# Performance work log

Measured on AMD Instinct MI355X. Metric: run time of the kernel, lower is better.

Reference implementation:

```python
import jax, jax.numpy as jnp
import numpy as np
from jax import lax

B, C1, C2, OUT, H, W = 8, 256, 128, 256, 64, 64
MID = max(C1, C2)
D = max(MID // 8, 4)

def conv1x1(x, w, b=None):
    # x: [B,C,H,W], w: [O,C]
    y = jnp.einsum('bchw,oc->bohw', x, w)
    if b is not None:
        y = y + b[None, :, None, None]
    return y

def dwconv3x3(x, w, b):
    # depthwise 3x3, padding=1; w: [C,1,3,3]
    y = lax.conv_general_dilated(x, w, (1, 1), 'SAME',
                                 dimension_numbers=('NCHW', 'OIHW', 'NCHW'),
                                 feature_group_count=x.shape[1])
    return y + b[None, :, None, None]

def setup_inputs() -> dict:
    key = jax.random.key(0)
    ks = jax.random.split(key, 16)
    def w1x1(k, o, i):
        return jax.random.normal(k, (o, i), jnp.float32) * np.sqrt(2.0 / o)
    def wdw(k, c):
        return jax.random.normal(k, (c, 1, 3, 3), jnp.float32) * np.sqrt(2.0 / (9 * c))
    z = lambda c: jnp.zeros((c,), jnp.float32)
    return {
        'x1': jax.random.normal(ks[0], (B, C1, H, W), jnp.float32),
        'x2': jax.random.normal(ks[1], (B, C2, H, W), jnp.float32),
        'conv_r_w': w1x1(ks[2], MID, C1), 'conv_r_b': z(MID),
        'conv_n_w': w1x1(ks[3], MID, C2), 'conv_n_b': z(MID),
        'mlp_w1': w1x1(ks[4], D, MID),
        'mlp_w2': w1x1(ks[5], 2 * MID, D),
        'pq_w': w1x1(ks[6], MID, MID), 'pq_b': z(MID),
        'dq_w': wdw(ks[7], MID), 'dq_b': z(MID),
        'pk_w': w1x1(ks[8], MID, MID), 'pk_b': z(MID),
        'dk_w': wdw(ks[9], MID), 'dk_b': z(MID),
        'pv_w': w1x1(ks[10], MID, MID), 'pv_b': z(MID),
        'dv_w': wdw(ks[11], MID), 'dv_b': z(MID),
        'out_w': w1x1(ks[12], OUT, MID), 'out_b': z(OUT),
        'alpha': jnp.float32(1.0),
        'lambd': jnp.float32(0.5),
        'beta': jnp.float32(0.5),
    }

def reference(x1, x2, conv_r_w, conv_r_b, conv_n_w, conv_n_b, mlp_w1, mlp_w2,
              pq_w, pq_b, dq_w, dq_b, pk_w, pk_b, dk_w, dk_b,
              pv_w, pv_b, dv_w, dv_b, out_w, out_b, alpha, lambd, beta):
    FR = conv1x1(x1, conv_r_w, conv_r_b)          # [B,C,H,W]
    FN = conv1x1(x2, conv_n_w, conv_n_b)          # [B,C,H,W]
    stack = jnp.stack([FR, FN], axis=1)           # [B,2,C,H,W]
    feats_sum = FR + FN
    pooled = feats_sum.mean(axis=(2, 3))          # [B,C] (adaptive avg pool 1x1)
    h = jax.nn.relu(jnp.einsum('bc,dc->bd', pooled, mlp_w1))
    a = jnp.einsum('bd,ed->be', h, mlp_w2).reshape(B, 2, MID)
    attn = jax.nn.softmax(a, axis=1)              # softmax over the 2 branches
    Fw = jnp.einsum('bkchw,bkc->bchw', stack, attn)
    Q = dwconv3x3(conv1x1(Fw, pq_w, pq_b), dq_w, dq_b)
    K = dwconv3x3(conv1x1(Fw, pk_w, pk_b), dk_w, dk_b)
    V = dwconv3x3(conv1x1(Fw, pv_w, pv_b), dv_w, dv_b)
    FQ = jnp.fft.fft2(Q.astype(jnp.float32), axes=(-2, -1))   # complex64 [B,C,H,W]
    FK = jnp.fft.fft2(K.astype(jnp.float32), axes=(-2, -1))
    elem = (FQ * FK).reshape(B, MID, H * W)                    # [B,C,HW]
    FQf = FQ.reshape(B, MID, H * W)
    FKf = FK.reshape(B, MID, H * W)
    attn_matrix = jnp.einsum('bcn,bdn->bcd', FQf, FKf)         # complex [B,C,C]
    attn_w = jax.nn.softmax(jnp.abs(attn_matrix) / alpha, axis=-1)
    attn_wc = attn_w.astype(jnp.complex64)
    F_CFR = jnp.einsum('bcd,bdn->bcn', attn_wc, elem).reshape(B, MID, H, W)
    cfr = jnp.real(jnp.fft.ifft2(F_CFR, axes=(-2, -1))).astype(Q.dtype)
    F_DFR = V - lambd * V * cfr
    freq_out = Q * cfr + F_DFR
    output = beta * freq_out + (1.0 - beta) * Fw
    return conv1x1(output, out_w, out_b)
```

## Files before the change

kernel.cpp:

```cpp
#include <hip/hip_runtime.h>
#include <math.h>

#ifndef M_PI
#define M_PI 3.14159265358979323846
#endif

typedef unsigned int u32;

constexpr int  NB   = 8;
constexpr int  CH   = 256;
constexpr long HW   = 4096;
constexpr long SLOT = (long)NB * CH * HW;
constexpr int  SPLITK = 8;
constexpr long ST   = (long)CH * HW;

__device__ __forceinline__ float rne_hi(float x) {
  unsigned u = __float_as_uint(x);
  unsigned r = (u + 0x7FFFu + ((u >> 16) & 1u)) & 0xFFFF0000u;
  return __uint_as_float(r);
}
__device__ __forceinline__ u32 packf(float x) {
  const float h = rne_hi(x);
  const float l = x - h;
  return (__float_as_uint(h) & 0xFFFF0000u) | (__float_as_uint(l) >> 16);
}
__device__ __forceinline__ float unpackf(u32 u) {
  return __uint_as_float(u & 0xFFFF0000u) + __uint_as_float(u << 16);
}
__device__ __forceinline__ unsigned bfpair(float x, float y) {
  return (__float_as_uint(x) >> 16) | (__float_as_uint(y) & 0xFFFF0000u);
}

typedef short bf16x8 __attribute__((ext_vector_type(8)));
typedef float f32x4  __attribute__((ext_vector_type(4)));

__global__ __launch_bounds__(256)
void cvt_kernel(const float* __restrict__ src, u32* __restrict__ dst, int n4)
{
  const int i = blockIdx.x * 256 + threadIdx.x;
  if (i < n4) {
    const float4 v = ((const float4*)src)[i];
    uint4 o;
    o.x = packf(v.x); o.y = packf(v.y); o.z = packf(v.z); o.w = packf(v.w);
    ((uint4*)dst)[i] = o;
  }
}

template<bool BPACKED, int EPI>
__global__ __launch_bounds__(256)
void gemm_mfma(const u32* __restrict__ A, const void* __restrict__ Bv,
               void* __restrict__ Cv, const float* __restrict__ bias,
               int K, long aStride, long bStride, long cStride,
               const u32* __restrict__ qb, const u32* __restrict__ vb,
               const u32* __restrict__ fwb,
               const float* __restrict__ lambd, const float* __restrict__ beta)
{
  constexpr int N = 4096;
  __shared__ __align__(16) unsigned short sAh[128 * 48];
  __shared__ __align__(16) unsigned short sAl[128 * 48];
  __shared__ __align__(16) unsigned short sBh[128 * 48];
  __shared__ __align__(16) unsigned short sBl[128 * 48];

  const int tid = threadIdx.x;
  const int b   = blockIdx.z;
  const int m0  = blockIdx.y * 128;
  const int n0  = blockIdx.x * 128;
  const u32* Ab = A + (long)b * aStride;

  const int ar = tid >> 1;
  const int ak = (tid & 1) * 16;
  const int aBase = ar * 48 + ak;
  const int bn = tid & 127;
  const int bk = (tid >> 7) * 16;
  const int bBase = bn * 48 + bk;

  const int wv = tid >> 6, lane = tid & 63;
  const int wy = wv >> 1, wx = wv & 1;
  const int quad = lane >> 4, l15 = lane & 15;

  f32x4 acc[4][4];
#pragma unroll
  for (int i = 0; i < 4; ++i)
#pragma unroll
    for (int j = 0; j < 4; ++j) acc[i][j] = (f32x4){0.f, 0.f, 0.f, 0.f};

  u32   ra[16];
  u32   rbu[16];
  float rbf[16];
  {
    const u32* ap = Ab + (long)(m0 + ar) * K + ak;
#pragma unroll
    for (int i = 0; i < 4; ++i) {
      const uint4 t = *(const uint4*)(ap + i * 4);
      ra[4*i] = t.x; ra[4*i+1] = t.y; ra[4*i+2] = t.z; ra[4*i+3] = t.w;
    }
    if (BPACKED) {
      const u32* bp = (const u32*)Bv + (long)b * bStride + (long)bk * N + n0 + bn;
#pragma unroll
      for (int i = 0; i < 16; ++i) rbu[i] = bp[(long)i * N];
    } else {
      const float* bp = (const float*)Bv + (long)b * bStride + (long)bk * N + n0 + bn;
#pragma unroll
      for (int i = 0; i < 16; ++i) rbf[i] = bp[(long)i * N];
    }
  }

  for (int kt = 0; kt < K; kt += 32) {
    {
      u32 hi[8], lo[8];
#pragma unroll
      for (int e = 0; e < 8; ++e) {
        const u32 u0 = ra[2*e], u1 = ra[2*e+1];
        hi[e] = (u0 >> 16) | (u1 & 0xFFFF0000u);
        lo[e] = (u0 & 0xFFFFu) | (u1 << 16);
      }
      *(uint4*)&sAh[aBase]     = make_uint4(hi[0], hi[1], hi[2], hi[3]);
      *(uint4*)&sAh[aBase + 8] = make_uint4(hi[4], hi[5], hi[6], hi[7]);
      *(uint4*)&sAl[aBase]     = make_uint4(lo[0], lo[1], lo[2], lo[3]);
      *(uint4*)&sAl[aBase + 8] = make_uint4(lo[4], lo[5], lo[6], lo[7]);
    }
    if (BPACKED) {
      u32 hi[8], lo[8];
#pragma unroll
      for (int e = 0; e < 8; ++e) {
        const u32 u0 = rbu[2*e], u1 = rbu[2*e+1];
        hi[e] = (u0 >> 16) | (u1 & 0xFFFF0000u);
        lo[e] = (u0 & 0xFFFFu) | (u1 << 16);
      }
      *(uint4*)&sBh[bBase]     = make_uint4(hi[0], hi[1], hi[2], hi[3]);
      *(uint4*)&sBh[bBase + 8] = make_uint4(hi[4], hi[5], hi[6], hi[7]);
      *(uint4*)&sBl[bBase]     = make_uint4(lo[0], lo[1], lo[2], lo[3]);
      *(uint4*)&sBl[bBase + 8] = make_uint4(lo[4], lo[5], lo[6], lo[7]);
    } else {
      float h[16], l[16];
#pragma unroll
      for (int e = 0; e < 16; ++e) { h[e] = rne_hi(rbf[e]); l[e] = rbf[e] - h[e]; }
      *(uint4*)&sBh[bBase]     = make_uint4(bfpair(h[0],h[1]), bfpair(h[2],h[3]),
                                            bfpair(h[4],h[5]), bfpair(h[6],h[7]));
      *(uint4*)&sBh[bBase + 8] = make_uint4(bfpair(h[8],h[9]), bfpair(h[10],h[11]),
                                            bfpair(h[12],h[13]), bfpair(h[14],h[15]));
      *(uint4*)&sBl[bBase]     = make_uint4(bfpair(l[0],l[1]), bfpair(l[2],l[3]),
                                            bfpair(l[4],l[5]), bfpair(l[6],l[7]));
      *(uint4*)&sBl[bBase + 8] = make_uint4(bfpair(l[8],l[9]), bfpair(l[10],l[11]),
                                            bfpair(l[12],l[13]), bfpair(l[14],l[15]));
    }
    __syncthreads();

    if (kt + 32 < K) {
      const u32* ap = Ab + (long)(m0 + ar) * K + kt + 32 + ak;
#pragma unroll
      for (int i = 0; i < 4; ++i) {
        const uint4 t = *(const uint4*)(ap + i * 4);
        ra[4*i] = t.x; ra[4*i+1] = t.y; ra[4*i+2] = t.z; ra[4*i+3] = t.w;
      }
      if (BPACKED) {
        const u32* bp = (const u32*)Bv + (long)b * bStride + (long)(kt + 32 + bk) * N + n0 + bn;
#pragma unroll
        for (int i = 0; i < 16; ++i) rbu[i] = bp[(long)i * N];
      } else {
        const float* bp = (const float*)Bv + (long)b * bStride + (long)(kt + 32 + bk) * N + n0 + bn;
#pragma unroll
        for (int i = 0; i < 16; ++i) rbf[i] = bp[(long)i * N];
      }
    }

    bf16x8 ah[4], al[4];
#pragma unroll
    for (int i = 0; i < 4; ++i) {
      const int idx = (wy * 64 + i * 16 + l15) * 48 + quad * 8;
      ah[i] = *(const bf16x8*)&sAh[idx];
      al[i] = *(const bf16x8*)&sAl[idx];
    }
#pragma unroll
    for (int j = 0; j < 4; ++j) {
      const int idx = (wx * 64 + j * 16 + l15) * 48 + quad * 8;
      const bf16x8 bh = *(const bf16x8*)&sBh[idx];
      const bf16x8 bl = *(const bf16x8*)&sBl[idx];
#pragma unroll
      for (int i = 0; i < 4; ++i) {
        acc[i][j] = __builtin_amdgcn_mfma_f32_16x16x32_bf16(ah[i], bh, acc[i][j], 0, 0, 0);
        acc[i][j] = __builtin_amdgcn_mfma_f32_16x16x32_bf16(ah[i], bl, acc[i][j], 0, 0, 0);
        acc[i][j] = __builtin_amdgcn_mfma_f32_16x16x32_bf16(al[i], bh, acc[i][j], 0, 0, 0);
      }
    }
    __syncthreads();
  }

  if (EPI == 0) {
    float* Cb = (float*)Cv + (long)b * cStride;
#pragma unroll
    for (int i = 0; i < 4; ++i)
#pragma unroll
      for (int r = 0; r < 4; ++r) {
        const int row = m0 + wy * 64 + i * 16 + quad * 4 + r;
        const float bb = bias ? bias[row] : 0.f;
#pragma unroll
        for (int j = 0; j < 4; ++j) {
          const int col = n0 + wx * 64 + j * 16 + l15;
          Cb[(long)row * N + col] = acc[i][j][r] + bb;
        }
      }
  } else if (EPI == 1) {
    u32* Cb = (u32*)Cv + (long)b * cStride;
#pragma unroll
    for (int i = 0; i < 4; ++i)
#pragma unroll
      for (int r = 0; r < 4; ++r) {
        const int row = m0 + wy * 64 + i * 16 + quad * 4 + r;
        const float bb = bias ? bias[row] : 0.f;
#pragma unroll
        for (int j = 0; j < 4; ++j) {
          const int col = n0 + wx * 64 + j * 16 + l15;
          Cb[(long)row * N + col] = packf(acc[i][j][r] + bb);
        }
      }
  } else {
    u32* Cb = (u32*)Cv + (long)b * cStride;
    const float lam = lambd[0], bet = beta[0];
#pragma unroll
    for (int i = 0; i < 4; ++i)
#pragma unroll
      for (int r = 0; r < 4; ++r) {
        const int row = m0 + wy * 64 + i * 16 + quad * 4 + r;
#pragma unroll
        for (int j = 0; j < 4; ++j) {
          const int col = n0 + wx * 64 + j * 16 + l15;
          const long off = (long)row * N + col;
          const long gi  = (long)b * cStride + off;
          const float q = unpackf(qb[gi]);
          const float v = unpackf(vb[gi]);
          const float f = unpackf(fwb[gi]);
          Cb[off] = packf(bet * (acc[i][j][r] * (q - lam * v) + v) + (1.f - bet) * f);
        }
      }
  }
}

__global__ __launch_bounds__(256)
void gemm_logits(const u32* __restrict__ Q, const u32* __restrict__ Kr,
                 float* __restrict__ Lp)
{
  __shared__ __align__(16) unsigned short sAh[128 * 48];
  __shared__ __align__(16) unsigned short sAl[128 * 48];
  __shared__ __align__(16) unsigned short sBh[128 * 48];
  __shared__ __align__(16) unsigned short sBl[128 * 48];

  const int tid = threadIdx.x;
  const int bz  = blockIdx.z;
  const int b   = bz >> 3, sp = bz & 7;
  const int m0  = blockIdx.y * 128;
  const int n0  = blockIdx.x * 128;
  const long k0b = (long)sp * 512;

  const int ar = tid >> 1;
  const int ak = (tid & 1) * 16;
  const int aBase = ar * 48 + ak;

  const int wv = tid >> 6, lane = tid & 63;
  const int wy = wv >> 1, wx = wv & 1;
  const int quad = lane >> 4, l15 = lane & 15;

  f32x4 acc[4][4];
#pragma unroll
  for (int i = 0; i < 4; ++i)
#pragma unroll
    for (int j = 0; j < 4; ++j) acc[i][j] = (f32x4){0.f, 0.f, 0.f, 0.f};

  const u32* Abase = Q  + (long)b * ST + (long)(m0 + ar) * 4096 + k0b + ak;
  const u32* Bbase = Kr + (long)b * ST + (long)(n0 + ar) * 4096 + k0b + ak;

  u32 ra[16], rb[16];
#pragma unroll
  for (int i = 0; i < 4; ++i) {
    uint4 t = *(const uint4*)(Abase + i * 4);
    ra[4*i] = t.x; ra[4*i+1] = t.y; ra[4*i+2] = t.z; ra[4*i+3] = t.w;
    t = *(const uint4*)(Bbase + i * 4);
    rb[4*i] = t.x; rb[4*i+1] = t.y; rb[4*i+2] = t.z; rb[4*i+3] = t.w;
  }

  for (int kt = 0; kt < 512; kt += 32) {
    {
      u32 hi[8], lo[8];
#pragma unroll
      for (int e = 0; e < 8; ++e) {
        const u32 u0 = ra[2*e], u1 = ra[2*e+1];
        hi[e] = (u0 >> 16) | (u1 & 0xFFFF0000u);
        lo[e] = (u0 & 0xFFFFu) | (u1 << 16);
      }
      *(uint4*)&sAh[aBase]     = make_uint4(hi[0], hi[1], hi[2], hi[3]);
      *(uint4*)&sAh[aBase + 8] = make_uint4(hi[4], hi[5], hi[6], hi[7]);
      *(uint4*)&sAl[aBase]     = make_uint4(lo[0], lo[1], lo[2], lo[3]);
      *(uint4*)&sAl[aBase + 8] = make_uint4(lo[4], lo[5], lo[6], lo[7]);
#pragma unroll
      for (int e = 0; e < 8; ++e) {
        const u32 u0 = rb[2*e], u1 = rb[2*e+1];
        hi[e] = (u0 >> 16) | (u1 & 0xFFFF0000u);
        lo[e] = (u0 & 0xFFFFu) | (u1 << 16);
      }
      *(uint4*)&sBh[aBase]     = make_uint4(hi[0], hi[1], hi[2], hi[3]);
      *(uint4*)&sBh[aBase + 8] = make_uint4(hi[4], hi[5], hi[6], hi[7]);
      *(uint4*)&sBl[aBase]     = make_uint4(lo[0], lo[1], lo[2], lo[3]);
      *(uint4*)&sBl[aBase + 8] = make_uint4(lo[4], lo[5], lo[6], lo[7]);
    }
    __syncthreads();

    if (kt + 32 < 512) {
#pragma unroll
      for (int i = 0; i < 4; ++i) {
        uint4 t = *(const uint4*)(Abase + kt + 32 + i * 4);
        ra[4*i] = t.x; ra[4*i+1] = t.y; ra[4*i+2] = t.z; ra[4*i+3] = t.w;
        t = *(const uint4*)(Bbase + kt + 32 + i * 4);
        rb[4*i] = t.x; rb[4*i+1] = t.y; rb[4*i+2] = t.z; rb[4*i+3] = t.w;
      }
    }

    bf16x8 ah[4], al[4];
#pragma unroll
    for (int i = 0; i < 4; ++i) {
      const int idx = (wy * 64 + i * 16 + l15) * 48 + quad * 8;
      ah[i] = *(const bf16x8*)&sAh[idx];
      al[i] = *(const bf16x8*)&sAl[idx];
    }
#pragma unroll
    for (int j = 0; j < 4; ++j) {
      const int idx = (wx * 64 + j * 16 + l15) * 48 + quad * 8;
      const bf16x8 bh = *(const bf16x8*)&sBh[idx];
      const bf16x8 bl = *(const bf16x8*)&sBl[idx];
#pragma unroll
      for (int i = 0; i < 4; ++i) {
        acc[i][j] = __builtin_amdgcn_mfma_f32_16x16x32_bf16(ah[i], bh, acc[i][j], 0, 0, 0);
        acc[i][j] = __builtin_amdgcn_mfma_f32_16x16x32_bf16(ah[i], bl, acc[i][j], 0, 0, 0);
        acc[i][j] = __builtin_amdgcn_mfma_f32_16x16x32_bf16(al[i], bh, acc[i][j], 0, 0, 0);
      }
    }
    __syncthreads();
  }

  float* Lb = Lp + (long)bz * 65536;
#pragma unroll
  for (int i = 0; i < 4; ++i)
#pragma unroll
    for (int r = 0; r < 4; ++r) {
      const int row = m0 + wy * 64 + i * 16 + quad * 4 + r;
#pragma unroll
      for (int j = 0; j < 4; ++j) {
        const int col = n0 + wx * 64 + j * 16 + l15;
        Lb[(long)row * 256 + col] = acc[i][j][r];
      }
    }
}

__global__ __launch_bounds__(256)
void pool_kernel(const u32* __restrict__ FR, const u32* __restrict__ FN,
                 float* __restrict__ pooled)
{
  __shared__ float red[256];
  const int bc = blockIdx.x, tid = threadIdx.x;
  const uint4* a = (const uint4*)(FR + (long)bc * HW);
  const uint4* b = (const uint4*)(FN + (long)bc * HW);
  float s = 0.f;
  for (int v = tid; v < 1024; v += 256) {
    const uint4 x = a[v];
    s += unpackf(x.x) + unpackf(x.y) + unpackf(x.z) + unpackf(x.w);
    const uint4 y = b[v];
    s += unpackf(y.x) + unpackf(y.y) + unpackf(y.z) + unpackf(y.w);
  }
  red[tid] = s; __syncthreads();
  for (int o = 128; o > 0; o >>= 1) {
    if (tid < o) red[tid] += red[tid + o];
    __syncthreads();
  }
  if (tid == 0) pooled[bc] = red[0] * (1.f / 4096.f);
}

__global__ __launch_bounds__(256)
void attn2_kernel(const float* __restrict__ pooled, const float* __restrict__ w1,
                  const float* __restrict__ w2, float* __restrict__ attn2)
{
  __shared__ float ps[256];
  __shared__ float hs[32];
  const int b = blockIdx.x, tid = threadIdx.x;
  ps[tid] = pooled[b * 256 + tid];
  __syncthreads();
  if (tid < 32) {
    float a = 0.f;
    for (int c = 0; c < 256; ++c) a += ps[c] * w1[tid * 256 + c];
    hs[tid] = fmaxf(a, 0.f);
  }
  __syncthreads();
  float a0 = 0.f, a1 = 0.f;
  for (int d = 0; d < 32; ++d) {
    const float h = hs[d];
    a0 += h * w2[tid * 32 + d];
    a1 += h * w2[(256 + tid) * 32 + d];
  }
  const float m  = fmaxf(a0, a1);
  const float e0 = expf(a0 - m), e1 = expf(a1 - m);
  const float inv = 1.f / (e0 + e1);
  attn2[b * 512 + tid]       = e0 * inv;
  attn2[b * 512 + 256 + tid] = e1 * inv;
}

__global__ __launch_bounds__(256)
void fw_kernel(const u32* __restrict__ FR, const u32* __restrict__ FN,
               const float* __restrict__ attn2, u32* __restrict__ FW)
{
  const int b = blockIdx.z, c = blockIdx.y;
  const float a0 = attn2[b * 512 + c];
  const float a1 = attn2[b * 512 + 256 + c];
  const long base4 = ((long)b * 256 + c) * 1024;
  const int i = blockIdx.x * 256 + threadIdx.x;
  const uint4 r = ((const uint4*)FR)[base4 + i];
  const uint4 n = ((const uint4*)FN)[base4 + i];
  uint4 o;
  o.x = packf(a0 * unpackf(r.x) + a1 * unpackf(n.x));
  o.y = packf(a0 * unpackf(r.y) + a1 * unpackf(n.y));
  o.z = packf(a0 * unpackf(r.z) + a1 * unpackf(n.z));
  o.w = packf(a0 * unpackf(r.w) + a1 * unpackf(n.w));
  ((uint4*)FW)[base4 + i] = o;
}

__global__ __launch_bounds__(256)
void dw_kernel(const u32* __restrict__ in, const float* __restrict__ w,
               const float* __restrict__ bias, u32* __restrict__ out,
               u32* __restrict__ out_rev)
{
  __shared__ float img[66][66];
  const int bc = blockIdx.x, tid = threadIdx.x;
  const int c = bc & 255;
  for (int v = tid; v < 66 * 66; v += 256) ((float*)img)[v] = 0.f;
  __syncthreads();
  const uint4* in4 = (const uint4*)(in + (long)bc * HW);
  for (int v = tid; v < 1024; v += 256) {
    const uint4 x = in4[v];
    const int r = v >> 4, c0 = ((v & 15) << 2) + 1;
    img[r + 1][c0 + 0] = unpackf(x.x);
    img[r + 1][c0 + 1] = unpackf(x.y);
    img[r + 1][c0 + 2] = unpackf(x.z);
    img[r + 1][c0 + 3] = unpackf(x.w);
  }
  float wr[9];
#pragma unroll
  for (int j = 0; j < 9; ++j) wr[j] = w[c * 9 + j];
  const float bb = bias[c];
  __syncthreads();
  for (int p = tid; p < 4096; p += 256) {
    const int y = p >> 6, x = p & 63;
    float s = bb;
#pragma unroll
    for (int ky = 0; ky < 3; ++ky)
#pragma unroll
      for (int kx = 0; kx < 3; ++kx)
        s = fmaf(wr[ky * 3 + kx], img[y + ky][x + kx], s);
    const u32 u = packf(s);
    out[(long)bc * HW + p] = u;
    if (out_rev)
      out_rev[(long)bc * HW + (((64 - y) & 63) << 6) + ((64 - x) & 63)] = u;
  }
}

#define SWA(r, c) (((r) << 6) | ((c) ^ (r)))
#define REV6(x)   ((((x) & 3) << 4) | ((x) & 12) | ((x) >> 4))

__device__ __forceinline__ float2 cmul(float2 a, float2 w) {
  return make_float2(a.x * w.x - a.y * w.y, a.x * w.y + a.y * w.x);
}
__device__ __forceinline__ float2 cmulc(float2 a, float2 w) {
  return make_float2(a.x * w.x + a.y * w.y, a.y * w.x - a.x * w.y);
}

__device__ __forceinline__ void fft_fwd(float2* __restrict__ Z,
                                        const float2* __restrict__ twt, int tid)
{
  const int lane = tid & 63;
  const int kb   = tid >> 6;
  for (int pass = 0; pass < 2; ++pass) {
    for (int s = 0; s < 3; ++s) {
      const int h  = 1 << (2 * s);
      const int us = 16 >> (2 * s);
#pragma unroll
      for (int q = 0; q < 4; ++q) {
        const int k = kb + 4 * q;
        const int j = k & (h - 1);
        const int g = k >> (2 * s);
        const int bse = g * 4 * h + j;
        const int p0 = bse, p1 = bse + h, p2 = bse + 2 * h, p3 = bse + 3 * h;
        const int a0 = pass ? SWA(p0, lane) : SWA(lane, p0);
        const int a1 = pass ? SWA(p1, lane) : SWA(lane, p1);
        const int a2 = pass ? SWA(p2, lane) : SWA(lane, p2);
        const int a3 = pass ? SWA(p3, lane) : SWA(lane, p3);
        float2 x0 = Z[a0];
        float2 x1 = Z[a1];
        float2 x2 = Z[a2];
        float2 x3 = Z[a3];
        const int e = j * us;
        x1 = cmul(x1, twt[e & 63]);
        x2 = cmul(x2, twt[(2 * e) & 63]);
        x3 = cmul(x3, twt[(3 * e) & 63]);
        const float2 t0 = make_float2(x0.x + x2.x, x0.y + x2.y);
        const float2 t1 = make_float2(x0.x - x2.x, x0.y - x2.y);
        const float2 t2 = make_float2(x1.x + x3.x, x1.y + x3.y);
        const float2 t3 = make_float2(x1.x - x3.x, x1.y - x3.y);
        Z[a0] = make_float2(t0.x + t2.x, t0.y + t2.y);
        Z[a2] = make_float2(t0.x - t2.x, t0.y - t2.y);
        Z[a1] = make_float2(t1.x + t3.y, t1.y - t3.x);
        Z[a3] = make_float2(t1.x - t3.y, t1.y + t3.x);
      }
      __syncthreads();
    }
  }
}

__device__ __forceinline__ void fft_inv(float2* __restrict__ Z,
                                        const float2* __restrict__ twt, int tid)
{
  const int lane = tid & 63;
  const int kb   = tid >> 6;
  for (int pass = 0; pass < 2; ++pass) {
    for (int s = 2; s >= 0; --s) {
      const int h  = 1 << (2 * s);
      const int us = 16 >> (2 * s);
#pragma unroll
      for (int q = 0; q < 4; ++q) {
        const int k = kb + 4 * q;
        const int j = k & (h - 1);
        const int g = k >> (2 * s);
        const int bse = g * 4 * h + j;
        const int p0 = bse, p1 = bse + h, p2 = bse + 2 * h, p3 = bse + 3 * h;
        const int a0 = pass ? SWA(lane, p0) : SWA(p0, lane);
        const int a1 = pass ? SWA(lane, p1) : SWA(p1, lane);
        const int a2 = pass ? SWA(lane, p2) : SWA(p2, lane);
        const int a3 = pass ? SWA(lane, p3) : SWA(p3, lane);
        const float2 x0 = Z[a0];
        const float2 x1 = Z[a1];
        const float2 x2 = Z[a2];
        const float2 x3 = Z[a3];
        const float2 t0 = make_float2(x0.x + x2.x, x0.y + x2.y);
        const float2 t1 = make_float2(x0.x - x2.x, x0.y - x2.y);
        const float2 t2 = make_float2(x1.x + x3.x, x1.y + x3.y);
        const float2 t3 = make_float2(x1.x - x3.x, x1.y - x3.y);
        const float2 y0 = make_float2(t0.x + t2.x, t0.y + t2.y);
        float2 y2 = make_float2(t0.x - t2.x, t0.y - t2.y);
        float2 y1 = make_float2(t1.x - t3.y, t1.y + t3.x);
        float2 y3 = make_float2(t1.x + t3.y, t1.y - t3.x);
        const int e = j * us;
        y1 = cmulc(y1, twt[e & 63]);
        y2 = cmulc(y2, twt[(2 * e) & 63]);
        y3 = cmulc(y3, twt[(3 * e) & 63]);
        Z[a0] = y0;
        Z[a1] = y1;
        Z[a2] = y2;
        Z[a3] = y3;
      }
      __syncthreads();
    }
  }
}

__global__ __launch_bounds__(256, 4)
void sconv_kernel(const u32* __restrict__ Qg, const u32* __restrict__ Kg,
                  u32* __restrict__ Sg)
{
  __shared__ float2 Z[4096];
  __shared__ float2 twt[64];
  const int tid = threadIdx.x;
  const long base = (long)blockIdx.x * 4096;
  if (tid < 64) {
    float sn, cs;
    __sincosf(-2.f * (float)M_PI * (float)tid * (1.f / 64.f), &sn, &cs);
    twt[tid] = make_float2(cs, sn);
  }

  {
    const uint4* Q4 = (const uint4*)(Qg + base);
    const uint4* K4 = (const uint4*)(Kg + base);
#pragma unroll
    for (int i = 0; i < 4; ++i) {
      const int v = tid + 256 * i;
      const uint4 q = Q4[v], k = K4[v];
      const int r = v >> 4, w = v & 15;
      const int R  = REV6(r);
      const int cb = ((w & 3) << 2) | (w >> 2);
      Z[SWA(R, cb)]      = make_float2(unpackf(q.x), unpackf(k.x));
      Z[SWA(R, cb + 16)] = make_float2(unpackf(q.y), unpackf(k.y));
      Z[SWA(R, cb + 32)] = make_float2(unpackf(q.z), unpackf(k.z));
      Z[SWA(R, cb + 48)] = make_float2(unpackf(q.w), unpackf(k.w));
    }
  }
  __syncthreads();

  fft_fwd(Z, twt, tid);

#pragma unroll
  for (int i = 0; i < 9; ++i) {
    const int n = tid + 256 * i;
    if (n < 2112) {
      const int u = n >> 6, vv = n & 63;
      if (!((u == 0 || u == 32) && vv > 32)) {
        const int u2 = (64 - u) & 63, v2 = (64 - vv) & 63;
        const int az = SWA(u, vv), am = SWA(u2, v2);
        const float2 z = Z[az];
        const float2 m = Z[am];
        const float dre = 0.25f * (z.x * z.x - z.y * z.y - m.x * m.x + m.y * m.y);
        const float dim = 0.5f  * (z.x * z.y + m.x * m.y);
        Z[az] = make_float2(dim, -dre);
        Z[am] = make_float2(dim,  dre);
      }
    }
  }
  __syncthreads();

  fft_inv(Z, twt, tid);

  uint4* S4 = (uint4*)(Sg + base);
#pragma unroll
  for (int i = 0; i < 4; ++i) {
    const int v = tid + 256 * i;
    const int y = v >> 4, w = v & 15;
    const int Rr = REV6(y);
    const int cb = ((w & 3) << 2) | (w >> 2);
    uint4 o;
    o.x = packf(Z[SWA(Rr, cb)].x      * (1.f / 4096.f));
    o.y = packf(Z[SWA(Rr, cb + 16)].x * (1.f / 4096.f));
    o.z = packf(Z[SWA(Rr, cb + 32)].x * (1.f / 4096.f));
    o.w = packf(Z[SWA(Rr, cb + 48)].x * (1.f / 4096.f));
    S4[v] = o;
  }
}

__global__ __launch_bounds__(256)
void softmax_kernel(const float* __restrict__ Lp, u32* __restrict__ L,
                    const float* __restrict__ alpha)
{
  __shared__ float red[256];
  const int row = blockIdx.x, tid = threadIdx.x;
  const int b = row >> 8, c = row & 255;
  const float sc = 4096.f / alpha[0];
  float acc = 0.f;
#pragma unroll
  for (int s = 0; s < SPLITK; ++s)
    acc += Lp[((long)(b * SPLITK + s) * 65536) + (long)c * 256 + tid];
  const float v = fabsf(acc) * sc;
  red[tid] = v; __syncthreads();
  for (int o = 128; o > 0; o >>= 1) {
    if (tid < o) red[tid] = fmaxf(red[tid], red[tid + o]);
    __syncthreads();
  }
  const float mx = red[0];
  __syncthreads();
  const float e = expf(v - mx);
  red[tid] = e; __syncthreads();
  for (int o = 128; o > 0; o >>= 1) {
    if (tid < o) red[tid] += red[tid + o];
    __syncthreads();
  }
  L[(long)row * 256 + tid] = packf(e / red[0]);
}

extern "C" void kernel_launch(void* const* d_in, const int* in_sizes, int n_in,
                              void* d_out, int out_size, void* d_ws, size_t ws_size,
                              hipStream_t stream)
{
  const float* x1       = (const float*)d_in[0];
  const float* x2       = (const float*)d_in[1];
  const float* conv_r_w = (const float*)d_in[2];
  const float* conv_r_b = (const float*)d_in[3];
  const float* conv_n_w = (const float*)d_in[4];
  const float* conv_n_b = (const float*)d_in[5];
  const float* mlp_w1   = (const float*)d_in[6];
  const float* mlp_w2   = (const float*)d_in[7];
  const float* pq_w     = (const float*)d_in[8];
  const float* pq_b     = (const float*)d_in[9];
  const float* dq_w     = (const float*)d_in[10];
  const float* dq_b     = (const float*)d_in[11];
  const float* pk_w     = (const float*)d_in[12];
  const float* pk_b     = (const float*)d_in[13];
  const float* dk_w     = (const float*)d_in[14];
  const float* dk_b     = (const float*)d_in[15];
  const float* pv_w     = (const float*)d_in[16];
  const float* pv_b     = (const float*)d_in[17];
  const float* dv_w     = (const float*)d_in[18];
  const float* dv_b     = (const float*)d_in[19];
  const float* out_w    = (const float*)d_in[20];
  const float* out_b    = (const float*)d_in[21];
  const float* alpha    = (const float*)d_in[22];
  const float* lambd    = (const float*)d_in[23];
  const float* beta     = (const float*)d_in[24];

  u32* s = (u32*)d_ws;
  u32* S0 = s;
  u32* S1 = s + SLOT;
  u32* S2 = s + 2 * SLOT;
  u32* S3 = s + 3 * SLOT;
  u32* S4 = s + 4 * SLOT;
  u32* S5 = s + 5 * SLOT;
  float* Lp     = (float*)(s + 6 * SLOT);
  u32*   Lb     = (u32*)(Lp + (long)8 * SPLITK * 65536);
  float* pooled = (float*)(Lb + (long)8 * 65536);
  float* attn2  = pooled + 2048;
  u32*   wR     = (u32*)(attn2 + 4096);
  u32*   wN     = wR + 65536;
  u32*   wQ     = wN + 32768;
  u32*   wK     = wQ + 65536;
  u32*   wV     = wK + 65536;
  u32*   wO     = wV + 65536;

  const size_t needed =
      (size_t)(6 * SLOT + (long)8 * SPLITK * 65536 + 8L * 65536 + 2048 + 4096
               + 65536 * 5 + 32768) * 4;
  if (ws_size < needed) return;

  const long ST2 = (long)128 * HW;
  const long STL = (long)256 * 256;
  const dim3 gBig(32, 2, 8);

  cvt_kernel<<<64, 256, 0, stream>>>(conv_r_w, wR, 16384);
  cvt_kernel<<<32, 256, 0, stream>>>(conv_n_w, wN, 8192);
  cvt_kernel<<<64, 256, 0, stream>>>(pq_w, wQ, 16384);
  cvt_kernel<<<64, 256, 0, stream>>>(pk_w, wK, 16384);
  cvt_kernel<<<64, 256, 0, stream>>>(pv_w, wV, 16384);
  cvt_kernel<<<64, 256, 0, stream>>>(out_w, wO, 16384);

  gemm_mfma<false, 1><<<gBig, 256, 0, stream>>>(wR, x1, S0, conv_r_b,
      256, 0L, ST, ST, nullptr, nullptr, nullptr, nullptr, nullptr);
  gemm_mfma<false, 1><<<gBig, 256, 0, stream>>>(wN, x2, S1, conv_n_b,
      128, 0L, ST2, ST, nullptr, nullptr, nullptr, nullptr, nullptr);

  pool_kernel<<<2048, 256, 0, stream>>>(S0, S1, pooled);
  attn2_kernel<<<8, 256, 0, stream>>>(pooled, mlp_w1, mlp_w2, attn2);
  fw_kernel<<<dim3(4, 256, 8), 256, 0, stream>>>(S0, S1, attn2, S2);

  gemm_mfma<true, 1><<<gBig, 256, 0, stream>>>(wQ, S2, S3, pq_b,
      256, 0L, ST, ST, nullptr, nullptr, nullptr, nullptr, nullptr);
  gemm_mfma<true, 1><<<gBig, 256, 0, stream>>>(wK, S2, S4, pk_b,
      256, 0L, ST, ST, nullptr, nullptr, nullptr, nullptr, nullptr);
  gemm_mfma<true, 1><<<gBig, 256, 0, stream>>>(wV, S2, S5, pv_b,
      256, 0L, ST, ST, nullptr, nullptr, nullptr, nullptr, nullptr);

  dw_kernel<<<2048, 256, 0, stream>>>(S3, dq_w, dq_b, S0, nullptr);
  dw_kernel<<<2048, 256, 0, stream>>>(S4, dk_w, dk_b, S1, S3);
  dw_kernel<<<2048, 256, 0, stream>>>(S5, dv_w, dv_b, S4, nullptr);

  sconv_kernel<<<2048, 256, 0, stream>>>(S0, S1, S5);

  gemm_logits<<<dim3(2, 2, 64), 256, 0, stream>>>(S0, S3, Lp);
  softmax_kernel<<<2048, 256, 0, stream>>>(Lp, Lb, alpha);

  gemm_mfma<true, 2><<<gBig, 256, 0, stream>>>(Lb, S5, S2, nullptr,
      256, STL, ST, ST, S0, S4, S2, lambd, beta);

  gemm_mfma<true, 0><<<gBig, 256, 0, stream>>>(wO, S2, d_out, out_b,
      256, 0L, ST, ST, nullptr, nullptr, nullptr, nullptr, nullptr);
}
```

Before: 452.7 us.

## Fuse first two radix-4 FFT stages in registers and preload twiddles

After: 448.1 us. About the same (-1.0%).

```diff
diff --git a/kernel.cpp b/kernel.cpp
--- a/kernel.cpp
+++ b/kernel.cpp
@@ -468,102 +468,136 @@
 __device__ __forceinline__ float2 cmulc(float2 a, float2 w) {
   return make_float2(a.x * w.x + a.y * w.y, a.y * w.x - a.x * w.y);
 }
+__device__ __forceinline__ void r4fwd(float2& x0, float2& x1, float2& x2, float2& x3) {
+  const float2 t0 = make_float2(x0.x + x2.x, x0.y + x2.y);
+  const float2 t1 = make_float2(x0.x - x2.x, x0.y - x2.y);
+  const float2 t2 = make_float2(x1.x + x3.x, x1.y + x3.y);
+  const float2 t3 = make_float2(x1.x - x3.x, x1.y - x3.y);
+  x0 = make_float2(t0.x + t2.x, t0.y + t2.y);
+  x2 = make_float2(t0.x - t2.x, t0.y - t2.y);
+  x1 = make_float2(t1.x + t3.y, t1.y - t3.x);
+  x3 = make_float2(t1.x - t3.y, t1.y + t3.x);
+}
+__device__ __forceinline__ void r4inv(float2& x0, float2& x1, float2& x2, float2& x3) {
+  const float2 t0 = make_float2(x0.x + x2.x, x0.y + x2.y);
+  const float2 t1 = make_float2(x0.x - x2.x, x0.y - x2.y);
+  const float2 t2 = make_float2(x1.x + x3.x, x1.y + x3.y);
+  const float2 t3 = make_float2(x1.x - x3.x, x1.y - x3.y);
+  x0 = make_float2(t0.x + t2.x, t0.y + t2.y);
+  x2 = make_float2(t0.x - t2.x, t0.y - t2.y);
+  x1 = make_float2(t1.x - t3.y, t1.y + t3.x);
+  x3 = make_float2(t1.x + t3.y, t1.y - t3.x);
+}
 
 __device__ __forceinline__ void fft_fwd(float2* __restrict__ Z,
-                                        const float2* __restrict__ twt, int tid)
-{
-  const int lane = tid & 63;
-  const int kb   = tid >> 6;
+                                        const float2 (&wA)[3][3],
+                                        const float2 (&wB)[4][3],
+                                        int lane, int kb)
+{
   for (int pass = 0; pass < 2; ++pass) {
-    for (int s = 0; s < 3; ++s) {
-      const int h  = 1 << (2 * s);
-      const int us = 16 >> (2 * s);
-#pragma unroll
-      for (int q = 0; q < 4; ++q) {
-        const int k = kb + 4 * q;
-        const int j = k & (h - 1);
-        const int g = k >> (2 * s);
-        const int bse = g * 4 * h + j;
-        const int p0 = bse, p1 = bse + h, p2 = bse + 2 * h, p3 = bse + 3 * h;
-        const int a0 = pass ? SWA(p0, lane) : SWA(lane, p0);
-        const int a1 = pass ? SWA(p1, lane) : SWA(lane, p1);
-        const int a2 = pass ? SWA(p2, lane) : SWA(lane, p2);
-        const int a3 = pass ? SWA(p3, lane) : SWA(lane, p3);
-        float2 x0 = Z[a0];
-        float2 x1 = Z[a1];
-        float2 x2 = Z[a2];
-        float2 x3 = Z[a3];
-        const int e = j * us;
-        x1 = cmul(x1, twt[e & 63]);
-        x2 = cmul(x2, twt[(2 * e) & 63]);
-        x3 = cmul(x3, twt[(3 * e) & 63]);
-        const float2 t0 = make_float2(x0.x + x2.x, x0.y + x2.y);
-        const float2 t1 = make_float2(x0.x - x2.x, x0.y - x2.y);
-        const float2 t2 = make_float2(x1.x + x3.x, x1.y + x3.y);
-        const float2 t3 = make_float2(x1.x - x3.x, x1.y - x3.y);
-        Z[a0] = make_float2(t0.x + t2.x, t0.y + t2.y);
-        Z[a2] = make_float2(t0.x - t2.x, t0.y - t2.y);
-        Z[a1] = make_float2(t1.x + t3.y, t1.y - t3.x);
-        Z[a3] = make_float2(t1.x - t3.y, t1.y + t3.x);
-      }
-      __syncthreads();
-    }
+    {
+      float2 x[16];
+#pragma unroll
+      for (int m = 0; m < 16; ++m) {
+        const int p = 16 * kb + m;
+        x[m] = Z[pass ? SWA(p, lane) : SWA(lane, p)];
+      }
+#pragma unroll
+      for (int c = 0; c < 4; ++c)
+        r4fwd(x[4*c], x[4*c+1], x[4*c+2], x[4*c+3]);
+#pragma unroll
+      for (int j = 0; j < 4; ++j) {
+        if (j) {
+          x[j+4]  = cmul(x[j+4],  wA[j-1][0]);
+          x[j+8]  = cmul(x[j+8],  wA[j-1][1]);
+          x[j+12] = cmul(x[j+12], wA[j-1][2]);
+        }
+        r4fwd(x[j], x[j+4], x[j+8], x[j+12]);
+      }
+#pragma unroll
+      for (int m = 0; m < 16; ++m) {
+        const int p = 16 * kb + m;
+        Z[pass ? SWA(p, lane) : SWA(lane, p)] = x[m];
+      }
+    }
+    __syncthreads();
+#pragma unroll
+    for (int q = 0; q < 4; ++q) {
+      const int k = kb + 4 * q;
+      const int a0 = pass ? SWA(k,      lane) : SWA(lane, k);
+      const int a1 = pass ? SWA(k + 16, lane) : SWA(lane, k + 16);
+      const int a2 = pass ? SWA(k + 32, lane) : SWA(lane, k + 32);
+      const int a3 = pass ? SWA(k + 48, lane) : SWA(lane, k + 48);
+      float2 x0 = Z[a0], x1 = Z[a1], x2 = Z[a2], x3 = Z[a3];
+      x1 = cmul(x1, wB[q][0]);
+      x2 = cmul(x2, wB[q][1]);
+      x3 = cmul(x3, wB[q][2]);
+      r4fwd(x0, x1, x2, x3);
+      Z[a0] = x0; Z[a1] = x1; Z[a2] = x2; Z[a3] = x3;
+    }
+    __syncthreads();
   }
 }
 
 __device__ __forceinline__ void fft_inv(float2* __restrict__ Z,
-                                        const float2* __restrict__ twt, int tid)
-{
-  const int lane = tid & 63;
-  const int kb   = tid >> 6;
+                                        const float2 (&wA)[3][3],
+                                        const float2 (&wB)[4][3],
+                                        int lane, int kb)
+{
   for (int pass = 0; pass < 2; ++pass) {
-    for (int s = 2; s >= 0; --s) {
-      const int h  = 1 << (2 * s);
-      const int us = 16 >> (2 * s);
-#pragma unroll
-      for (int q = 0; q < 4; ++q) {
-        const int k = kb + 4 * q;
-        const int j = k & (h - 1);
-        const int g = k >> (2 * s);
-        const int bse = g * 4 * h + j;
-        const int p0 = bse, p1 = bse + h, p2 = bse + 2 * h, p3 = bse + 3 * h;
-        const int a0 = pass ? SWA(lane, p0) : SWA(p0, lane);
-        const int a1 = pass ? SWA(lane, p1) : SWA(p1, lane);
-        const int a2 = pass ? SWA(lane, p2) : SWA(p2, lane);
-        const int a3 = pass ? SWA(lane, p3) : SWA(p3, lane);
-        const float2 x0 = Z[a0];
-        const float2 x1 = Z[a1];
-        const float2 x2 = Z[a2];
-        const float2 x3 = Z[a3];
-        const float2 t0 = make_float2(x0.x + x2.x, x0.y + x2.y);
-        const float2 t1 = make_float2(x0.x - x2.x, x0.y - x2.y);
-        const float2 t2 = make_float2(x1.x + x3.x, x1.y + x3.y);
-        const float2 t3 = make_float2(x1.x - x3.x, x1.y - x3.y);
-        const float2 y0 = make_float2(t0.x + t2.x, t0.y + t2.y);
-        float2 y2 = make_float2(t0.x - t2.x, t0.y - t2.y);
-        float2 y1 = make_float2(t1.x - t3.y, t1.y + t3.x);
-        float2 y3 = make_float2(t1.x + t3.y, t1.y - t3.x);
-        const int e = j * us;
-        y1 = cmulc(y1, twt[e & 63]);
-        y2 = cmulc(y2, twt[(2 * e) & 63]);
-        y3 = cmulc(y3, twt[(3 * e) & 63]);
-        Z[a0] = y0;
-        Z[a1] = y1;
-        Z[a2] = y2;
-        Z[a3] = y3;
-      }
-      __syncthreads();
-    }
-  }
-}
-
-__global__ __launch_bounds__(256, 4)
+#pragma unroll
+    for (int q = 0; q < 4; ++q) {
+      const int k = kb + 4 * q;
+      const int a0 = pass ? SWA(lane, k)      : SWA(k,      lane);
+      const int a1 = pass ? SWA(lane, k + 16) : SWA(k + 16, lane);
+      const int a2 = pass ? SWA(lane, k + 32) : SWA(k + 32, lane);
+      const int a3 = pass ? SWA(lane, k + 48) : SWA(k + 48, lane);
+      float2 x0 = Z[a0], x1 = Z[a1], x2 = Z[a2], x3 = Z[a3];
+      r4inv(x0, x1, x2, x3);
+      x1 = cmulc(x1, wB[q][0]);
+      x2 = cmulc(x2, wB[q][1]);
+      x3 = cmulc(x3, wB[q][2]);
+      Z[a0] = x0; Z[a1] = x1; Z[a2] = x2; Z[a3] = x3;
+    }
+    __syncthreads();
+    {
+      float2 x[16];
+#pragma unroll
+      for (int m = 0; m < 16; ++m) {
+        const int p = 16 * kb + m;
+        x[m] = Z[pass ? SWA(lane, p) : SWA(p, lane)];
+      }
+#pragma unroll
+      for (int j = 0; j < 4; ++j) {
+        r4inv(x[j], x[j+4], x[j+8], x[j+12]);
+        if (j) {
+          x[j+4]  = cmulc(x[j+4],  wA[j-1][0]);
+          x[j+8]  = cmulc(x[j+8],  wA[j-1][1]);
+          x[j+12] = cmulc(x[j+12], wA[j-1][2]);
+        }
+      }
+#pragma unroll
+      for (int c = 0; c < 4; ++c)
+        r4inv(x[4*c], x[4*c+1], x[4*c+2], x[4*c+3]);
+#pragma unroll
+      for (int m = 0; m < 16; ++m) {
+        const int p = 16 * kb + m;
+        Z[pass ? SWA(lane, p) : SWA(p, lane)] = x[m];
+      }
+    }
+    __syncthreads();
+  }
+}
+
+__global__ __launch_bounds__(256, 3)
 void sconv_kernel(const u32* __restrict__ Qg, const u32* __restrict__ Kg,
                   u32* __restrict__ Sg)
 {
   __shared__ float2 Z[4096];
   __shared__ float2 twt[64];
   const int tid = threadIdx.x;
+  const int lane = tid & 63;
+  const int kb   = tid >> 6;
   const long base = (long)blockIdx.x * 4096;
   if (tid < 64) {
     float sn, cs;
@@ -589,7 +623,22 @@
   }
   __syncthreads();
 
-  fft_fwd(Z, twt, tid);
+  float2 wA[3][3], wB[4][3];
+#pragma unroll
+  for (int j = 1; j < 4; ++j) {
+    wA[j-1][0] = twt[(4  * j) & 63];
+    wA[j-1][1] = twt[(8  * j) & 63];
+    wA[j-1][2] = twt[(12 * j) & 63];
+  }
+#pragma unroll
+  for (int q = 0; q < 4; ++q) {
+    const int k = kb + 4 * q;
+    wB[q][0] = twt[k];
+    wB[q][1] = twt[(2 * k) & 63];
+    wB[q][2] = twt[(3 * k) & 63];
+  }
+
+  fft_fwd(Z, wA, wB, lane, kb);
 
 #pragma unroll
   for (int i = 0; i < 9; ++i) {
@@ -610,7 +659,7 @@
   }
   __syncthreads();
 
-  fft_inv(Z, twt, tid);
+  fft_inv(Z, wA, wB, lane, kb);
 
   uint4* S4 = (uint4*)(Sg + base);
 #pragma unroll
```
